# Kernel optimization log

Hardware: AMD Instinct MI355X
Metric: run time of the kernel (lower is better)

Reference implementation:

```python
import jax, jax.numpy as jnp
import numpy as np

BS, T, N, M = 2048, 128, 256, 256


def setup_inputs() -> dict:
    key = jax.random.key(0)
    ks = jax.random.split(key, 8)
    s = 0.05
    return {
        "x": jax.random.normal(ks[0], (BS, T, N), dtype=jnp.float32),
        "W_e": jax.random.normal(ks[1], (T, 2 * M), dtype=jnp.float32) * s,
        "U_e": jax.random.normal(ks[2], (T, T), dtype=jnp.float32) * s,
        "V_e": jax.random.normal(ks[3], (1, T), dtype=jnp.float32) * s,
        "W_ih": jax.random.normal(ks[4], (4 * M, N), dtype=jnp.float32) * s,
        "W_hh": jax.random.normal(ks[5], (4 * M, M), dtype=jnp.float32) * s,
        "b_ih": jax.random.normal(ks[6], (4 * M,), dtype=jnp.float32) * s,
        "b_hh": jax.random.normal(ks[7], (4 * M,), dtype=jnp.float32) * s,
    }


def reference(x, W_e, U_e, V_e, W_ih, W_hh, b_ih, b_hh):
    bs = x.shape[0]
    t_len = U_e.shape[0]
    m = W_hh.shape[1]
    # U_e(x.permute(0,2,1)) is loop-invariant; hoist it: (bs, n, T)
    Ux = jnp.einsum('btn,st->bns', x, U_e)

    def step(carry, _):
        h, s = carry                                  # each (bs, m)
        hs = jnp.concatenate([h, s], axis=1)          # (bs, 2m)
        whs = hs @ W_e.T                              # (bs, T)
        tanh_sum = jnp.tanh(Ux + whs[:, None, :])     # (bs, n, T)
        e = jnp.einsum('bnt,t->bn', tanh_sum, V_e[0]) # (bs, n)
        alpha = jax.nn.softmax(e, axis=1)
        # faithful to source: x_t_tilde = alpha_t * e_t (NOT alpha_t * x_t)
        xt = alpha * e                                # (bs, n)
        gates = xt @ W_ih.T + b_ih + h @ W_hh.T + b_hh
        i, f, g, o = jnp.split(gates, 4, axis=1)
        c = jax.nn.sigmoid(f) * s + jax.nn.sigmoid(i) * jnp.tanh(g)
        h_new = jax.nn.sigmoid(o) * jnp.tanh(c)
        return (h_new, c), h_new

    init = (jnp.zeros((bs, m), x.dtype), jnp.zeros((bs, m), x.dtype))
    _, hs_all = jax.lax.scan(step, init, xs=None, length=t_len)  # (T, bs, m)
    return jnp.transpose(hs_all, (1, 2, 0))           # (bs, m, T)
```

## Files before the change

kernel.cpp:

```cpp
#include <hip/hip_runtime.h>
#include <stdint.h>

typedef short  s8v  __attribute__((ext_vector_type(8)));
typedef float  f4v  __attribute__((ext_vector_type(4)));
typedef int    i4v  __attribute__((ext_vector_type(4)));

#define MFMA16(a,b,c) __builtin_amdgcn_mfma_f32_16x16x32_bf16(a,b,c,0,0,0)

#define K1 1.44269504088896340f
#define K2 2.88539008177792681f

__device__ __forceinline__ unsigned short f2bf(float f) {
  union { float f; uint32_t u; } v; v.f = f;
  return (unsigned short)((v.u + 0x7FFFu + ((v.u >> 16) & 1u)) >> 16);
}
__device__ __forceinline__ float bflo(uint32_t dw) {
  union { uint32_t u; float f; } v; v.u = dw << 16; return v.f;
}
__device__ __forceinline__ float bfhi(uint32_t dw) {
  union { uint32_t u; float f; } v; v.u = dw & 0xFFFF0000u; return v.f;
}

__global__ __launch_bounds__(256) void prep_kernel(
    const float* __restrict__ We, const float* __restrict__ Ue,
    const float* __restrict__ Wih, const float* __restrict__ Whh,
    const float* __restrict__ bih, const float* __restrict__ bhh,
    unsigned short* __restrict__ Wih_b, unsigned short* __restrict__ Whh_b,
    unsigned short* __restrict__ We_b, unsigned short* __restrict__ Ue_b,
    float* __restrict__ bsum)
{
  int i0 = blockIdx.x * 256 + threadIdx.x;
  int stride = gridDim.x * 256;
  for (int i = i0; i < 262144; i += stride) Wih_b[i] = f2bf(Wih[i]);
  for (int i = i0; i < 262144; i += stride) Whh_b[i] = f2bf(Whh[i]);
  for (int i = i0; i < 65536;  i += stride) We_b[i]  = f2bf(We[i]);
  for (int i = i0; i < 16384;  i += stride) Ue_b[i]  = f2bf(Ue[i]);
  for (int i = i0; i < 1024;   i += stride) bsum[i]  = bih[i] + bhh[i];
}

__global__ __launch_bounds__(256) void ux_kernel(
    const float* __restrict__ x, const unsigned short* __restrict__ Ue_b,
    unsigned short* __restrict__ UxK)
{
  __shared__ unsigned short xT[64 * 136];
  __shared__ unsigned short oT[64 * 136];
  const int tid = threadIdx.x;
  const int b   = blockIdx.x >> 2;
  const int n0  = (blockIdx.x & 3) * 64;

  {
    const int nl = tid & 63, tp = tid >> 6;
    for (int i = 0; i < 32; i++) {
      int t = tp + i * 4;
      xT[nl * 136 + t] = f2bf(x[((size_t)b * 128 + t) * 256 + n0 + nl]);
    }
  }
  __syncthreads();
  {
    const int w = tid >> 6, lane = tid & 63;
    const int l15 = lane & 15, quad = lane >> 4;
    for (int tt = 0; tt < 8; tt++) {
      f4v acc = {0.f, 0.f, 0.f, 0.f};
      #pragma unroll
      for (int kt = 0; kt < 4; kt++) {
        s8v a  = *(const s8v*)&xT[(w * 16 + l15) * 136 + kt * 32 + quad * 8];
        s8v bb = *(const s8v*)&Ue_b[(tt * 16 + l15) * 128 + kt * 32 + quad * 8];
        acc = MFMA16(a, bb, acc);
      }
      #pragma unroll
      for (int r = 0; r < 4; r++)
        oT[(w * 16 + quad * 4 + r) * 136 + tt * 16 + l15] = f2bf(acc[r] * K2);
    }
  }
  __syncthreads();
  {
    for (int p = 0; p < 2; p++) {
      int row = (tid >> 3) + p * 32;
      int c16 = (tid & 7) * 16;
      const i4v* src = (const i4v*)&oT[row * 136 + c16];
      i4v* dst = (i4v*)&UxK[(((size_t)b * 256) + n0 + row) * 128 + c16];
      dst[0] = src[0];
      dst[1] = src[1];
    }
  }
}

__global__ __launch_bounds__(1024, 4) void rnn_kernel(
    const unsigned short* __restrict__ UxK,
    const unsigned short* __restrict__ We_b,
    const unsigned short* __restrict__ Wih_b,
    const unsigned short* __restrict__ Whh_b,
    const float* __restrict__ bsum_g,
    const float* __restrict__ Ve,
    float* __restrict__ out)
{
  __shared__ float  h_hist[8 * 256 * 8];
  __shared__ unsigned short xt_b[16 * 264];
  __shared__ unsigned short h_b [16 * 264];
  __shared__ unsigned short c_b [16 * 264];
  __shared__ float  c_f[8 * 256];
  __shared__ float  e_f[8 * 256];
  __shared__ float  wv_lds[8 * 128 * 2];
  __shared__ float  bsum[1024];
  __shared__ float  Zp[16];
  __shared__ float  Zi[8];

  const int tid  = threadIdx.x;
  const int wv   = tid >> 6;
  const int lane = tid & 63;
  const int l15  = lane & 15;
  const int quad = lane >> 4;

  for (int i = tid; i < 16 * 264; i += 1024) { xt_b[i] = 0; h_b[i] = 0; c_b[i] = 0; }
  for (int i = tid; i < 2048; i += 1024) c_f[i] = 0.f;
  bsum[tid] = bsum_g[tid];
  {
    int b8 = tid >> 7, t = tid & 127;
    wv_lds[(b8 * 128 + t) * 2 + 1] = -2.0f * Ve[t];
    wv_lds[(b8 * 128 + t) * 2 + 0] = 0.f;
  }
  float Vs = 0.f;
  for (int t = 0; t < 128; t++) Vs += Ve[t];
  __syncthreads();

  const int an = tid & 255;
  const int bq = tid >> 8;

  f4v ga0, ga1, ga2, ga3;

  for (int s = 0; s < 128; s++) {
    __syncthreads();

    if (wv < 8) {
      f4v acc = {0.f, 0.f, 0.f, 0.f};
      #pragma unroll
      for (int kt = 0; kt < 8; kt++) {
        s8v a  = *(const s8v*)&h_b[l15 * 264 + kt * 32 + quad * 8];
        s8v bb = *(const s8v*)&We_b[(wv * 16 + l15) * 512 + kt * 32 + quad * 8];
        acc = MFMA16(a, bb, acc);
      }
      #pragma unroll
      for (int kt = 0; kt < 8; kt++) {
        s8v a  = *(const s8v*)&c_b[l15 * 264 + kt * 32 + quad * 8];
        s8v bb = *(const s8v*)&We_b[(wv * 16 + l15) * 512 + 256 + kt * 32 + quad * 8];
        acc = MFMA16(a, bb, acc);
      }
      if (lane < 32) {
        #pragma unroll
        for (int r = 0; r < 4; r++)
          wv_lds[((quad * 4 + r) * 128 + wv * 16 + l15) * 2] = K2 * acc[r];
      }
    }
    __syncthreads();

    ga0 = (f4v){0.f,0.f,0.f,0.f}; ga1 = ga0; ga2 = ga0; ga3 = ga0;
    #pragma unroll
    for (int kt = 0; kt < 8; kt++) {
      s8v a = *(const s8v*)&h_b[l15 * 264 + kt * 32 + quad * 8];
      int ko = kt * 32 + quad * 8;
      s8v b0 = *(const s8v*)&Whh_b[(size_t)(  0 + wv * 16 + l15) * 256 + ko];
      s8v b1 = *(const s8v*)&Whh_b[(size_t)(256 + wv * 16 + l15) * 256 + ko];
      s8v b2 = *(const s8v*)&Whh_b[(size_t)(512 + wv * 16 + l15) * 256 + ko];
      s8v b3 = *(const s8v*)&Whh_b[(size_t)(768 + wv * 16 + l15) * 256 + ko];
      ga0 = MFMA16(a, b0, ga0);
      ga1 = MFMA16(a, b1, ga1);
      ga2 = MFMA16(a, b2, ga2);
      ga3 = MFMA16(a, b3, ga3);
    }

    #pragma unroll
    for (int pass = 0; pass < 2; pass++) {
      const int bb8 = bq + pass * 4;
      const i4v* up4 = (const i4v*)(UxK + (((size_t)blockIdx.x * 8 + bb8) * 256 + an) * 128);
      const float* wvp = &wv_lds[bb8 * 256];
      float acc0 = 0.f, acc1 = 0.f;
      #pragma unroll 4
      for (int tg = 0; tg < 16; tg++) {
        i4v d = up4[tg];
        #pragma unroll
        for (int q = 0; q < 4; q++) {
          uint32_t dw = (uint32_t)d[q];
          int t2 = (tg * 8 + q * 2) * 2;
          float2 p0 = *(const float2*)&wvp[t2];
          float2 p1 = *(const float2*)&wvp[t2 + 2];
          float x0 = bflo(dw) + p0.x;
          float r0 = __builtin_amdgcn_rcpf(__builtin_amdgcn_exp2f(x0) + 1.0f);
          acc0 = fmaf(p0.y, r0, acc0);
          float x1 = bfhi(dw) + p1.x;
          float r1 = __builtin_amdgcn_rcpf(__builtin_amdgcn_exp2f(x1) + 1.0f);
          acc1 = fmaf(p1.y, r1, acc1);
        }
      }
      e_f[bb8 * 256 + an] = Vs + acc0 + acc1;
    }
    __syncthreads();

    const int b8s = tid >> 7;
    const int nn0 = (tid & 127) * 2;
    float e0 = e_f[b8s * 256 + nn0];
    float e1 = e_f[b8s * 256 + nn0 + 1];
    float p0 = __builtin_amdgcn_exp2f(K1 * e0);
    float p1 = __builtin_amdgcn_exp2f(K1 * e1);
    float ssum = p0 + p1;
    #pragma unroll
    for (int off = 32; off >= 1; off >>= 1) ssum += __shfl_xor(ssum, off);
    if (lane == 0) Zp[wv] = ssum;
    __syncthreads();
    if (tid < 8) Zi[tid] = 1.0f / (Zp[2 * tid] + Zp[2 * tid + 1]);
    __syncthreads();
    {
      float zi = Zi[b8s];
      unsigned int packed = (unsigned int)f2bf(p0 * zi * e0)
                          | ((unsigned int)f2bf(p1 * zi * e1) << 16);
      *(unsigned int*)&xt_b[b8s * 264 + nn0] = packed;
    }
    __syncthreads();

    #pragma unroll
    for (int kt = 0; kt < 8; kt++) {
      s8v a = *(const s8v*)&xt_b[l15 * 264 + kt * 32 + quad * 8];
      int ko = kt * 32 + quad * 8;
      s8v b0 = *(const s8v*)&Wih_b[(size_t)(  0 + wv * 16 + l15) * 256 + ko];
      s8v b1 = *(const s8v*)&Wih_b[(size_t)(256 + wv * 16 + l15) * 256 + ko];
      s8v b2 = *(const s8v*)&Wih_b[(size_t)(512 + wv * 16 + l15) * 256 + ko];
      s8v b3 = *(const s8v*)&Wih_b[(size_t)(768 + wv * 16 + l15) * 256 + ko];
      ga0 = MFMA16(a, b0, ga0);
      ga1 = MFMA16(a, b1, ga1);
      ga2 = MFMA16(a, b2, ga2);
      ga3 = MFMA16(a, b3, ga3);
    }

    if (lane < 32) {
      const int jj = wv * 16 + l15;
      #pragma unroll
      for (int r = 0; r < 4; r++) {
        const int m = quad * 4 + r;
        float iG = ga0[r] + bsum[jj];
        float fG = ga1[r] + bsum[256 + jj];
        float gG = ga2[r] + bsum[512 + jj];
        float oG = ga3[r] + bsum[768 + jj];
        float si = __builtin_amdgcn_rcpf(1.0f + __builtin_amdgcn_exp2f(-K1 * iG));
        float sf = __builtin_amdgcn_rcpf(1.0f + __builtin_amdgcn_exp2f(-K1 * fG));
        float so = __builtin_amdgcn_rcpf(1.0f + __builtin_amdgcn_exp2f(-K1 * oG));
        float tg_ = 1.0f - 2.0f * __builtin_amdgcn_rcpf(1.0f + __builtin_amdgcn_exp2f(K2 * gG));
        float cn = sf * c_f[m * 256 + jj] + si * tg_;
        float th = 1.0f - 2.0f * __builtin_amdgcn_rcpf(1.0f + __builtin_amdgcn_exp2f(K2 * cn));
        float hn = so * th;
        c_f[m * 256 + jj] = cn;
        c_b[m * 264 + jj] = f2bf(cn);
        h_b[m * 264 + jj] = f2bf(hn);
        h_hist[(m * 256 + jj) * 8 + (s & 7)] = hn;
      }
    }

    if ((s & 7) == 7) {
      __syncthreads();
      #pragma unroll
      for (int p = 0; p < 2; p++) {
        int rid = p * 1024 + tid;
        int mB = rid >> 8, j = rid & 255;
        const f4v* src = (const f4v*)&h_hist[rid * 8];
        f4v* dst = (f4v*)&out[(((size_t)blockIdx.x * 8 + mB) * 256 + j) * 128 + (s - 7)];
        __builtin_nontemporal_store(src[0], dst);
        __builtin_nontemporal_store(src[1], dst + 1);
      }
    }
  }
}

extern "C" void kernel_launch(void* const* d_in, const int* in_sizes, int n_in,
                              void* d_out, int out_size, void* d_ws, size_t ws_size,
                              hipStream_t stream) {
  const float* x   = (const float*)d_in[0];
  const float* We  = (const float*)d_in[1];
  const float* Ue  = (const float*)d_in[2];
  const float* Ve  = (const float*)d_in[3];
  const float* Wih = (const float*)d_in[4];
  const float* Whh = (const float*)d_in[5];
  const float* bih = (const float*)d_in[6];
  const float* bhh = (const float*)d_in[7];
  float* out = (float*)d_out;

  char* p = (char*)d_ws;
  unsigned short* UxK   = (unsigned short*)p; p += (size_t)134217728;
  unsigned short* Wih_b = (unsigned short*)p; p += 524288;
  unsigned short* Whh_b = (unsigned short*)p; p += 524288;
  unsigned short* We_b  = (unsigned short*)p; p += 131072;
  unsigned short* Ue_b  = (unsigned short*)p; p += 32768;
  float* bsum = (float*)p;

  prep_kernel<<<512, 256, 0, stream>>>(We, Ue, Wih, Whh, bih, bhh,
                                       Wih_b, Whh_b, We_b, Ue_b, bsum);
  ux_kernel<<<8192, 256, 0, stream>>>(x, Ue_b, UxK);
  rnn_kernel<<<256, 1024, 0, stream>>>(UxK, We_b, Wih_b, Whh_b, bsum, Ve, out);
}
```

Measured before the change: 11.84 ms.

## Store Ux in FP8 with coalesced layout, fuse softmax partials, bf16 history

Ux is stored as FP8 in a time-group-major layout, which halves the per-step global read traffic and coalesces the loads. The loads are issued as nontemporal prefetches ahead of the Whh MFMA loop so they overlap with that compute. Softmax partial sums are computed inside the attention pass, removing one barrier and a separate reduction stage. The output history is kept in bf16 and flushed every 16 steps instead of 8, and the weight loads are unrolled in pairs. FP8 and bf16 history add precision loss that may exceed tolerance.

```diff
diff --git a/kernel.cpp b/kernel.cpp
--- a/kernel.cpp
+++ b/kernel.cpp
@@ -3,7 +3,9 @@
 
 typedef short  s8v  __attribute__((ext_vector_type(8)));
 typedef float  f4v  __attribute__((ext_vector_type(4)));
+typedef float  f2v  __attribute__((ext_vector_type(2)));
 typedef int    i4v  __attribute__((ext_vector_type(4)));
+typedef unsigned short us4 __attribute__((ext_vector_type(4)));
 
 #define MFMA16(a,b,c) __builtin_amdgcn_mfma_f32_16x16x32_bf16(a,b,c,0,0,0)
 
@@ -19,6 +21,9 @@
 }
 __device__ __forceinline__ float bfhi(uint32_t dw) {
   union { uint32_t u; float f; } v; v.u = dw & 0xFFFF0000u; return v.f;
+}
+__device__ __forceinline__ float bfu(unsigned short u) {
+  union { uint32_t u; float f; } v; v.u = ((uint32_t)u) << 16; return v.f;
 }
 
 __global__ __launch_bounds__(256) void prep_kernel(
@@ -40,7 +45,7 @@
 
 __global__ __launch_bounds__(256) void ux_kernel(
     const float* __restrict__ x, const unsigned short* __restrict__ Ue_b,
-    unsigned short* __restrict__ UxK)
+    unsigned char* __restrict__ UxK8)
 {
   __shared__ unsigned short xT[64 * 136];
   __shared__ unsigned short oT[64 * 136];
@@ -76,17 +81,23 @@
   {
     for (int p = 0; p < 2; p++) {
       int row = (tid >> 3) + p * 32;
-      int c16 = (tid & 7) * 16;
-      const i4v* src = (const i4v*)&oT[row * 136 + c16];
-      i4v* dst = (i4v*)&UxK[(((size_t)b * 256) + n0 + row) * 128 + c16];
-      dst[0] = src[0];
-      dst[1] = src[1];
+      int tg  = tid & 7;
+      const unsigned int* sp = (const unsigned int*)&oT[row * 136 + tg * 16];
+      i4v outv;
+      #pragma unroll
+      for (int j = 0; j < 4; j++) {
+        unsigned int d0 = sp[2 * j], d1 = sp[2 * j + 1];
+        int w = __builtin_amdgcn_cvt_pk_fp8_f32(bflo(d0), bfhi(d0), 0, 0);
+        w     = __builtin_amdgcn_cvt_pk_fp8_f32(bflo(d1), bfhi(d1), w, 1);
+        outv[j] = w;
+      }
+      *(i4v*)&UxK8[(((size_t)b * 8 + tg) * 256 + n0 + row) * 16] = outv;
     }
   }
 }
 
 __global__ __launch_bounds__(1024, 4) void rnn_kernel(
-    const unsigned short* __restrict__ UxK,
+    const unsigned char* __restrict__ UxK8,
     const unsigned short* __restrict__ We_b,
     const unsigned short* __restrict__ Wih_b,
     const unsigned short* __restrict__ Whh_b,
@@ -94,7 +105,7 @@
     const float* __restrict__ Ve,
     float* __restrict__ out)
 {
-  __shared__ float  h_hist[8 * 256 * 8];
+  __shared__ unsigned short h_hist[2048 * 20];
   __shared__ unsigned short xt_b[16 * 264];
   __shared__ unsigned short h_b [16 * 264];
   __shared__ unsigned short c_b [16 * 264];
@@ -102,14 +113,14 @@
   __shared__ float  e_f[8 * 256];
   __shared__ float  wv_lds[8 * 128 * 2];
   __shared__ float  bsum[1024];
-  __shared__ float  Zp[16];
-  __shared__ float  Zi[8];
+  __shared__ float  Zpart[8][4];
 
   const int tid  = threadIdx.x;
   const int wv   = tid >> 6;
   const int lane = tid & 63;
   const int l15  = lane & 15;
   const int quad = lane >> 4;
+  const int blk  = blockIdx.x;
 
   for (int i = tid; i < 16 * 264; i += 1024) { xt_b[i] = 0; h_b[i] = 0; c_b[i] = 0; }
   for (int i = tid; i < 2048; i += 1024) c_f[i] = 0.f;
@@ -126,6 +137,10 @@
   const int an = tid & 255;
   const int bq = tid >> 8;
 
+  const i4v* ub = (const i4v*)UxK8;
+  const size_t ux_base0 = ((size_t)(blk * 8 + bq)    ) * 2048 + an;
+  const size_t ux_base1 = ((size_t)(blk * 8 + bq + 4)) * 2048 + an;
+
   f4v ga0, ga1, ga2, ga3;
 
   for (int s = 0; s < 128; s++) {
@@ -153,81 +168,106 @@
     }
     __syncthreads();
 
+    i4v d0[8];
+    #pragma unroll
+    for (int tg = 0; tg < 8; tg++)
+      d0[tg] = __builtin_nontemporal_load(ub + ux_base0 + tg * 256);
+
     ga0 = (f4v){0.f,0.f,0.f,0.f}; ga1 = ga0; ga2 = ga0; ga3 = ga0;
     #pragma unroll
-    for (int kt = 0; kt < 8; kt++) {
-      s8v a = *(const s8v*)&h_b[l15 * 264 + kt * 32 + quad * 8];
-      int ko = kt * 32 + quad * 8;
-      s8v b0 = *(const s8v*)&Whh_b[(size_t)(  0 + wv * 16 + l15) * 256 + ko];
-      s8v b1 = *(const s8v*)&Whh_b[(size_t)(256 + wv * 16 + l15) * 256 + ko];
-      s8v b2 = *(const s8v*)&Whh_b[(size_t)(512 + wv * 16 + l15) * 256 + ko];
-      s8v b3 = *(const s8v*)&Whh_b[(size_t)(768 + wv * 16 + l15) * 256 + ko];
-      ga0 = MFMA16(a, b0, ga0);
-      ga1 = MFMA16(a, b1, ga1);
-      ga2 = MFMA16(a, b2, ga2);
-      ga3 = MFMA16(a, b3, ga3);
-    }
+    for (int kp = 0; kp < 4; kp++) {
+      const int k0 = kp * 2, k1 = kp * 2 + 1;
+      s8v aA = *(const s8v*)&h_b[l15 * 264 + k0 * 32 + quad * 8];
+      s8v aB = *(const s8v*)&h_b[l15 * 264 + k1 * 32 + quad * 8];
+      const int r0 = (wv * 16 + l15) * 256;
+      s8v b00 = *(const s8v*)&Whh_b[(size_t)(     0 + r0) + k0 * 32 + quad * 8];
+      s8v b01 = *(const s8v*)&Whh_b[(size_t)( 65536 + r0) + k0 * 32 + quad * 8];
+      s8v b02 = *(const s8v*)&Whh_b[(size_t)(131072 + r0) + k0 * 32 + quad * 8];
+      s8v b03 = *(const s8v*)&Whh_b[(size_t)(196608 + r0) + k0 * 32 + quad * 8];
+      s8v b10 = *(const s8v*)&Whh_b[(size_t)(     0 + r0) + k1 * 32 + quad * 8];
+      s8v b11 = *(const s8v*)&Whh_b[(size_t)( 65536 + r0) + k1 * 32 + quad * 8];
+      s8v b12 = *(const s8v*)&Whh_b[(size_t)(131072 + r0) + k1 * 32 + quad * 8];
+      s8v b13 = *(const s8v*)&Whh_b[(size_t)(196608 + r0) + k1 * 32 + quad * 8];
+      ga0 = MFMA16(aA, b00, ga0); ga1 = MFMA16(aA, b01, ga1);
+      ga2 = MFMA16(aA, b02, ga2); ga3 = MFMA16(aA, b03, ga3);
+      ga0 = MFMA16(aB, b10, ga0); ga1 = MFMA16(aB, b11, ga1);
+      ga2 = MFMA16(aB, b12, ga2); ga3 = MFMA16(aB, b13, ga3);
+    }
+
+    {
+      i4v d1[8];
+      #pragma unroll
+      for (int tg = 0; tg < 8; tg++)
+        d1[tg] = __builtin_nontemporal_load(ub + ux_base1 + tg * 256);
+
+      #pragma unroll
+      for (int pass = 0; pass < 2; pass++) {
+        const int bb8 = bq + pass * 4;
+        const f4v* wvf = (const f4v*)&wv_lds[bb8 * 256];
+        float a0 = 0.f, a1 = 0.f, a2 = 0.f, a3 = 0.f;
+        #pragma unroll
+        for (int tg = 0; tg < 8; tg++) {
+          i4v d = pass ? d1[tg] : d0[tg];
+          #pragma unroll
+          for (int q = 0; q < 4; q++) {
+            uint32_t dw = (uint32_t)d[q];
+            f2v lo = __builtin_amdgcn_cvt_pk_f32_fp8(dw, 0);
+            f2v hi = __builtin_amdgcn_cvt_pk_f32_fp8(dw, 1);
+            const int t = tg * 16 + q * 4;
+            f4v w01 = wvf[(t >> 1)];
+            f4v w23 = wvf[(t >> 1) + 1];
+            float x0 = lo.x + w01.x;
+            a0 = fmaf(w01.y, __builtin_amdgcn_rcpf(__builtin_amdgcn_exp2f(x0) + 1.0f), a0);
+            float x1 = lo.y + w01.z;
+            a1 = fmaf(w01.w, __builtin_amdgcn_rcpf(__builtin_amdgcn_exp2f(x1) + 1.0f), a1);
+            float x2 = hi.x + w23.x;
+            a2 = fmaf(w23.y, __builtin_amdgcn_rcpf(__builtin_amdgcn_exp2f(x2) + 1.0f), a2);
+            float x3 = hi.y + w23.z;
+            a3 = fmaf(w23.w, __builtin_amdgcn_rcpf(__builtin_amdgcn_exp2f(x3) + 1.0f), a3);
+          }
+        }
+        float e = Vs + ((a0 + a1) + (a2 + a3));
+        e_f[bb8 * 256 + an] = e;
+        float pe = __builtin_amdgcn_exp2f(K1 * e);
+        #pragma unroll
+        for (int off = 32; off >= 1; off >>= 1) pe += __shfl_xor(pe, off);
+        if (lane == 0) Zpart[bb8][wv & 3] = pe;
+      }
+    }
+    __syncthreads();
+
+    {
+      const int b8s = tid >> 7;
+      const int nn0 = (tid & 127) * 2;
+      f4v zp = *(const f4v*)&Zpart[b8s][0];
+      float zi = 1.0f / ((zp.x + zp.y) + (zp.z + zp.w));
+      float2 ee = *(const float2*)&e_f[b8s * 256 + nn0];
+      float p0 = __builtin_amdgcn_exp2f(K1 * ee.x);
+      float p1 = __builtin_amdgcn_exp2f(K1 * ee.y);
+      unsigned int packed = (unsigned int)f2bf(p0 * zi * ee.x)
+                          | ((unsigned int)f2bf(p1 * zi * ee.y) << 16);
+      *(unsigned int*)&xt_b[b8s * 264 + nn0] = packed;
+    }
+    __syncthreads();
 
     #pragma unroll
-    for (int pass = 0; pass < 2; pass++) {
-      const int bb8 = bq + pass * 4;
-      const i4v* up4 = (const i4v*)(UxK + (((size_t)blockIdx.x * 8 + bb8) * 256 + an) * 128);
-      const float* wvp = &wv_lds[bb8 * 256];
-      float acc0 = 0.f, acc1 = 0.f;
-      #pragma unroll 4
-      for (int tg = 0; tg < 16; tg++) {
-        i4v d = up4[tg];
-        #pragma unroll
-        for (int q = 0; q < 4; q++) {
-          uint32_t dw = (uint32_t)d[q];
-          int t2 = (tg * 8 + q * 2) * 2;
-          float2 p0 = *(const float2*)&wvp[t2];
-          float2 p1 = *(const float2*)&wvp[t2 + 2];
-          float x0 = bflo(dw) + p0.x;
-          float r0 = __builtin_amdgcn_rcpf(__builtin_amdgcn_exp2f(x0) + 1.0f);
-          acc0 = fmaf(p0.y, r0, acc0);
-          float x1 = bfhi(dw) + p1.x;
-          float r1 = __builtin_amdgcn_rcpf(__builtin_amdgcn_exp2f(x1) + 1.0f);
-          acc1 = fmaf(p1.y, r1, acc1);
-        }
-      }
-      e_f[bb8 * 256 + an] = Vs + acc0 + acc1;
-    }
-    __syncthreads();
-
-    const int b8s = tid >> 7;
-    const int nn0 = (tid & 127) * 2;
-    float e0 = e_f[b8s * 256 + nn0];
-    float e1 = e_f[b8s * 256 + nn0 + 1];
-    float p0 = __builtin_amdgcn_exp2f(K1 * e0);
-    float p1 = __builtin_amdgcn_exp2f(K1 * e1);
-    float ssum = p0 + p1;
-    #pragma unroll
-    for (int off = 32; off >= 1; off >>= 1) ssum += __shfl_xor(ssum, off);
-    if (lane == 0) Zp[wv] = ssum;
-    __syncthreads();
-    if (tid < 8) Zi[tid] = 1.0f / (Zp[2 * tid] + Zp[2 * tid + 1]);
-    __syncthreads();
-    {
-      float zi = Zi[b8s];
-      unsigned int packed = (unsigned int)f2bf(p0 * zi * e0)
-                          | ((unsigned int)f2bf(p1 * zi * e1) << 16);
-      *(unsigned int*)&xt_b[b8s * 264 + nn0] = packed;
-    }
-    __syncthreads();
-
-    #pragma unroll
-    for (int kt = 0; kt < 8; kt++) {
-      s8v a = *(const s8v*)&xt_b[l15 * 264 + kt * 32 + quad * 8];
-      int ko = kt * 32 + quad * 8;
-      s8v b0 = *(const s8v*)&Wih_b[(size_t)(  0 + wv * 16 + l15) * 256 + ko];
-      s8v b1 = *(const s8v*)&Wih_b[(size_t)(256 + wv * 16 + l15) * 256 + ko];
-      s8v b2 = *(const s8v*)&Wih_b[(size_t)(512 + wv * 16 + l15) * 256 + ko];
-      s8v b3 = *(const s8v*)&Wih_b[(size_t)(768 + wv * 16 + l15) * 256 + ko];
-      ga0 = MFMA16(a, b0, ga0);
-      ga1 = MFMA16(a, b1, ga1);
-      ga2 = MFMA16(a, b2, ga2);
-      ga3 = MFMA16(a, b3, ga3);
+    for (int kp = 0; kp < 4; kp++) {
+      const int k0 = kp * 2, k1 = kp * 2 + 1;
+      s8v aA = *(const s8v*)&xt_b[l15 * 264 + k0 * 32 + quad * 8];
+      s8v aB = *(const s8v*)&xt_b[l15 * 264 + k1 * 32 + quad * 8];
+      const int r0 = (wv * 16 + l15) * 256;
+      s8v b00 = *(const s8v*)&Wih_b[(size_t)(     0 + r0) + k0 * 32 + quad * 8];
+      s8v b01 = *(const s8v*)&Wih_b[(size_t)( 65536 + r0) + k0 * 32 + quad * 8];
+      s8v b02 = *(const s8v*)&Wih_b[(size_t)(131072 + r0) + k0 * 32 + quad * 8];
+      s8v b03 = *(const s8v*)&Wih_b[(size_t)(196608 + r0) + k0 * 32 + quad * 8];
+      s8v b10 = *(const s8v*)&Wih_b[(size_t)(     0 + r0) + k1 * 32 + quad * 8];
+      s8v b11 = *(const s8v*)&Wih_b[(size_t)( 65536 + r0) + k1 * 32 + quad * 8];
+      s8v b12 = *(const s8v*)&Wih_b[(size_t)(131072 + r0) + k1 * 32 + quad * 8];
+      s8v b13 = *(const s8v*)&Wih_b[(size_t)(196608 + r0) + k1 * 32 + quad * 8];
+      ga0 = MFMA16(aA, b00, ga0); ga1 = MFMA16(aA, b01, ga1);
+      ga2 = MFMA16(aA, b02, ga2); ga3 = MFMA16(aA, b03, ga3);
+      ga0 = MFMA16(aB, b10, ga0); ga1 = MFMA16(aB, b11, ga1);
+      ga2 = MFMA16(aB, b12, ga2); ga3 = MFMA16(aB, b13, ga3);
     }
 
     if (lane < 32) {
@@ -249,20 +289,24 @@
         c_f[m * 256 + jj] = cn;
         c_b[m * 264 + jj] = f2bf(cn);
         h_b[m * 264 + jj] = f2bf(hn);
-        h_hist[(m * 256 + jj) * 8 + (s & 7)] = hn;
-      }
-    }
-
-    if ((s & 7) == 7) {
+        h_hist[(m * 256 + jj) * 20 + (s & 15)] = f2bf(hn);
+      }
+    }
+
+    if ((s & 15) == 15) {
       __syncthreads();
       #pragma unroll
       for (int p = 0; p < 2; p++) {
         int rid = p * 1024 + tid;
         int mB = rid >> 8, j = rid & 255;
-        const f4v* src = (const f4v*)&h_hist[rid * 8];
-        f4v* dst = (f4v*)&out[(((size_t)blockIdx.x * 8 + mB) * 256 + j) * 128 + (s - 7)];
-        __builtin_nontemporal_store(src[0], dst);
-        __builtin_nontemporal_store(src[1], dst + 1);
+        const us4* hp = (const us4*)&h_hist[rid * 20];
+        float* dst = &out[(((size_t)blk * 8 + mB) * 256 + j) * 128 + (s - 15)];
+        #pragma unroll
+        for (int c = 0; c < 4; c++) {
+          us4 u = hp[c];
+          f4v o = { bfu(u.x), bfu(u.y), bfu(u.z), bfu(u.w) };
+          __builtin_nontemporal_store(o, (f4v*)(dst + c * 4));
+        }
       }
     }
   }
@@ -282,7 +326,7 @@
   float* out = (float*)d_out;
 
   char* p = (char*)d_ws;
-  unsigned short* UxK   = (unsigned short*)p; p += (size_t)134217728;
+  unsigned char*  UxK8  = (unsigned char*)p;  p += (size_t)67108864;
   unsigned short* Wih_b = (unsigned short*)p; p += 524288;
   unsigned short* Whh_b = (unsigned short*)p; p += 524288;
   unsigned short* We_b  = (unsigned short*)p; p += 131072;
@@ -291,6 +335,6 @@
 
   prep_kernel<<<512, 256, 0, stream>>>(We, Ue, Wih, Whh, bih, bhh,
                                        Wih_b, Whh_b, We_b, Ue_b, bsum);
-  ux_kernel<<<8192, 256, 0, stream>>>(x, Ue_b, UxK);
-  rnn_kernel<<<256, 1024, 0, stream>>>(UxK, We_b, Wih_b, Whh_b, bsum, Ve, out);
-}
+  ux_kernel<<<8192, 256, 0, stream>>>(x, Ue_b, UxK8);
+  rnn_kernel<<<256, 1024, 0, stream>>>(UxK8, We_b, Wih_b, Whh_b, bsum, Ve, out);
+}
```

Result: slower. 16.44 ms (+38.9%).
